# Performance work log

Measured on AMD Instinct MI355X. Metric: run time of the kernel, lower is better.

## Reference

```python
import jax, jax.numpy as jnp
import numpy as np

ALPHA = 0.2   # curvature threshold (init arg alpha)
BETA = 0.5    # ODE step weight (init arg beta)
BIG = 1e9     # sentinel used by torch.where(den < alpha, 1e9, den)


def setup_inputs() -> dict:
    key = jax.random.key(0)
    ks = jax.random.split(key, 6)
    B, N, D = 8, 128, 256
    return {
        "node_inputs": jax.random.normal(ks[0], (B * N, D), jnp.float32),
        "edges_input": jax.random.normal(ks[1], (B * N * N, D), jnp.float32),
        "W_n2e": jax.random.normal(ks[2], (2 * D, D), jnp.float32) * 0.05,
        "b_n2e": jnp.zeros((D,), jnp.float32),
        "W_e2v1": jax.random.normal(ks[3], (D, D // 2), jnp.float32) * 0.05,
        "b_e2v1": jnp.zeros((D // 2,), jnp.float32),
        "W_e2v2": jax.random.normal(ks[4], (D // 2, 1), jnp.float32) * 0.05,
        "b_e2v2": jnp.zeros((1,), jnp.float32),
        "num_atoms": N,
    }


def calc_k(e):
    # e: [B, N, N] nonnegative edge values (relu output).
    # Faithful vectorization of the torch nonzero/scatter/max code:
    # for each masked edge (i, j), denominator = max over row (i resp. j) where
    # entries < alpha OR at columns {i, j} are replaced by 1e9 (the scattered
    # zeros are < alpha so they also become 1e9). We get the exact row max
    # excluding columns {i, j} from the per-row top-3, then max with BIG.
    B, N, _ = e.shape
    mask = (e >= ALPHA) & (e < 1.0)
    r = jnp.where(e < ALPHA, BIG, e)                 # [B, N, N]
    vals, idx = jax.lax.top_k(r, 3)                   # [B, N, 3]
    ar = jnp.arange(N)
    # den_i: uses row i's top-k; exclude entries at columns i (dim 1) and j (dim 2)
    excl_i = (idx[:, :, None, :] == ar[None, :, None, None]) | \
             (idx[:, :, None, :] == ar[None, None, :, None])   # [B, N, N, 3]
    den_i = jnp.maximum(
        jnp.max(jnp.where(excl_i, -jnp.inf, vals[:, :, None, :]), axis=-1), BIG)
    # den_j: uses row j's top-k; same column exclusions
    excl_j = (idx[:, None, :, :] == ar[None, :, None, None]) | \
             (idx[:, None, :, :] == ar[None, None, :, None])
    den_j = jnp.maximum(
        jnp.max(jnp.where(excl_j, -jnp.inf, vals[:, None, :, :]), axis=-1), BIG)
    num = jnp.where(mask, e, 1.0)  # safe value where unmasked (sqrt-grad safety)
    s = jnp.sqrt(num / den_i) + jnp.sqrt(num / den_j)
    cur = jnp.where(mask, s, 0.0)
    return 2.0 - cur.reshape(-1)                      # [B*N*N]


def reference(node_inputs, edges_input, W_n2e, b_n2e, W_e2v1, b_e2v1,
              W_e2v2, b_e2v2, num_atoms):
    N = num_atoms
    D = node_inputs.shape[1]
    x = node_inputs.reshape(-1, N, D)                 # [B, N, D]
    # rel_send/rel_rec one-hot matmuls == direct gathers (row-major edge order)
    send = jnp.arange(N * N) // N
    rec = jnp.arange(N * N) % N
    edges = jnp.concatenate([x[:, send, :], x[:, rec, :]], axis=-1)  # [B, N*N, 2D]
    ez = jax.nn.gelu(edges @ W_n2e + b_n2e, approximate=False)       # [B, N*N, D]
    # dropout p=0.0 -> identity
    h = jax.nn.relu(ez @ W_e2v1 + b_e2v1)             # [B, N*N, D/2]
    e2v = jax.nn.relu((h @ W_e2v2 + b_e2v2)[..., 0])  # [B, N*N]
    ez_flat = ez.reshape(-1, D)                       # [B*N*N, D]
    k = calc_k(e2v.reshape(-1, N, N))[:, None]        # [B*N*N, 1], broadcast over D
    sig = jax.nn.sigmoid(ez_flat)
    grad1 = (k - jnp.exp(sig)) * edges_input
    return ez_flat + BETA * grad1, e2v
```

## Files before the change

### kernel.cpp

```cpp
#include <hip/hip_runtime.h>
#include <cmath>

typedef __attribute__((ext_vector_type(8))) short bf16x8;
typedef __attribute__((ext_vector_type(4))) float f32x4;
typedef unsigned short u16;
typedef unsigned int u32;

#define OUT1OFF 33554432

__device__ __forceinline__ u16 f2bf(float f) {
  union { float f; u32 u; } v; v.f = f;
  u32 r = v.u + 0x7fffu + ((v.u >> 16) & 1u);
  return (u16)(r >> 16);
}

__device__ __forceinline__ float frcp(float x) {
  float r;
  asm("v_rcp_f32 %0, %1" : "=v"(r) : "v"(x));
  return r;
}

__device__ __forceinline__ u32 cvt_pk_bf16(float lo, float hi) {
  u32 r;
  asm("v_cvt_pk_bf16_f32 %0, %1, %2" : "=v"(r) : "v"(lo), "v"(hi));
  return r;
}

__device__ __forceinline__ float gelu_t(float x) {
  const float x2 = x * x;
  const float z = 1.5957691216057308f * x * fmaf(0.044715f, x2, 1.0f);
  return x * frcp(1.0f + __expf(-z));
}

__global__ __launch_bounds__(256) void k1_prep(
    const float* __restrict__ x, const float* __restrict__ Wn2e,
    const float* __restrict__ bn2e, const float* __restrict__ W1,
    float* __restrict__ Uw, float* __restrict__ Yw, u16* __restrict__ W1F)
{
  __shared__ float xl[4][256];
  const int t = threadIdx.x;
  const int blk = blockIdx.x;
  const int r0 = blk * 4;
  {
    const int rr = t >> 6, c4 = (t & 63) * 4;
    *(float4*)&xl[rr][c4] = *(const float4*)&x[(r0 + rr) * 256 + c4];
  }
  __syncthreads();
  const int c = t;
  float u0=0.f,u1=0.f,u2=0.f,u3=0.f,y0=0.f,y1=0.f,y2=0.f,y3=0.f;
  #pragma unroll 4
  for (int k = 0; k < 256; ++k) {
    const float wt = Wn2e[k * 256 + c];
    const float wb = Wn2e[(k + 256) * 256 + c];
    const float a0 = xl[0][k], a1 = xl[1][k], a2 = xl[2][k], a3 = xl[3][k];
    u0 = fmaf(a0, wt, u0); u1 = fmaf(a1, wt, u1);
    u2 = fmaf(a2, wt, u2); u3 = fmaf(a3, wt, u3);
    y0 = fmaf(a0, wb, y0); y1 = fmaf(a1, wb, y1);
    y2 = fmaf(a2, wb, y2); y3 = fmaf(a3, wb, y3);
  }
  const float bb = bn2e[c];
  Uw[(r0+0)*256+c]=u0; Uw[(r0+1)*256+c]=u1; Uw[(r0+2)*256+c]=u2; Uw[(r0+3)*256+c]=u3;
  Yw[(r0+0)*256+c]=y0+bb; Yw[(r0+1)*256+c]=y1+bb; Yw[(r0+2)*256+c]=y2+bb; Yw[(r0+3)*256+c]=y3+bb;
  if (blk < 64) {
    #pragma unroll
    for (int q = 0; q < 2; ++q) {
      const int e = (blk * 256 + t) * 2 + q;
      const int d = e & 7, lf = (e >> 3) & 63, ks = (e >> 9) & 7, nt = (e >> 12) & 7;
      const int n = nt * 16 + (lf & 15);
      const int kg = ks * 32 + ((lf >> 4) & 3) * 8 + d;
      W1F[e] = f2bf(W1[kg * 128 + n]);
    }
  }
}

__global__ __launch_bounds__(256, 4) void k2_fused(
    const float* __restrict__ Uw, const float* __restrict__ Yw,
    const u16* __restrict__ W1F, const float* __restrict__ b1,
    const float* __restrict__ W2, const float* __restrict__ b2p,
    const float* __restrict__ E, float* __restrict__ out)
{
  __shared__ u16 ezLds[64 * 256];
  const int t = threadIdx.x;
  const int blk = blockIdx.x;
  const int pair = blk >> 1;
  const int j0 = (blk & 1) * 64;
  const int b = pair >> 7;
  const int rw = t >> 6;
  const int c4 = (t & 63) * 4;

  const float4 uv = *(const float4*)&Uw[pair * 256 + c4];

  #pragma unroll 4
  for (int it = 0; it < 16; ++it) {
    const int jj = it * 4 + rw;
    const int g = pair * 128 + j0 + jj;
    const float4 yv = *(const float4*)&Yw[(b * 128 + j0 + jj) * 256 + c4];
    const float4 ev = *(const float4*)&E[g * 256 + c4];
    const float ez0 = gelu_t(uv.x + yv.x);
    const float ez1 = gelu_t(uv.y + yv.y);
    const float ez2 = gelu_t(uv.z + yv.z);
    const float ez3 = gelu_t(uv.w + yv.w);
    uint2 pk;
    pk.x = cvt_pk_bf16(ez0, ez1);
    pk.y = cvt_pk_bf16(ez2, ez3);
    const int idx = (jj * 256 + c4) ^ ((jj & 7) << 3);
    *(uint2*)&ezLds[idx] = pk;
    float4 o;
    o.x = ez0 + (1.f - 0.5f * __expf(frcp(1.f + __expf(-ez0)))) * ev.x;
    o.y = ez1 + (1.f - 0.5f * __expf(frcp(1.f + __expf(-ez1)))) * ev.y;
    o.z = ez2 + (1.f - 0.5f * __expf(frcp(1.f + __expf(-ez2)))) * ev.z;
    o.w = ez3 + (1.f - 0.5f * __expf(frcp(1.f + __expf(-ez3)))) * ev.w;
    *(float4*)&out[g * 256 + c4] = o;
  }
  __syncthreads();

  const int l = t & 63;
  const int l15 = l & 15, lh = l >> 4;
  const int m0 = rw * 16;
  f32x4 acc[8];
  #pragma unroll
  for (int nt = 0; nt < 8; ++nt) acc[nt] = (f32x4){0.f, 0.f, 0.f, 0.f};
  #pragma unroll
  for (int ks = 0; ks < 8; ++ks) {
    const int k = ks * 32 + lh * 8;
    const int aidx = ((m0 + l15) * 256 + k) ^ ((l15 & 7) << 3);
    const bf16x8 a = *(const bf16x8*)&ezLds[aidx];
    #pragma unroll
    for (int nt = 0; nt < 8; ++nt) {
      const bf16x8 bv = *(const bf16x8*)&W1F[(((nt << 3) | ks) * 64 + l) * 8];
      acc[nt] = __builtin_amdgcn_mfma_f32_16x16x32_bf16(a, bv, acc[nt], 0, 0, 0);
    }
  }
  float ps0=0.f, ps1=0.f, ps2=0.f, ps3=0.f;
  #pragma unroll
  for (int nt = 0; nt < 8; ++nt) {
    const int col = nt * 16 + l15;
    const float bv = b1[col], wvv = W2[col];
    ps0 += fmaxf(acc[nt][0] + bv, 0.f) * wvv;
    ps1 += fmaxf(acc[nt][1] + bv, 0.f) * wvv;
    ps2 += fmaxf(acc[nt][2] + bv, 0.f) * wvv;
    ps3 += fmaxf(acc[nt][3] + bv, 0.f) * wvv;
  }
  #pragma unroll
  for (int m = 1; m < 16; m <<= 1) {
    ps0 += __shfl_xor(ps0, m, 64);
    ps1 += __shfl_xor(ps1, m, 64);
    ps2 += __shfl_xor(ps2, m, 64);
    ps3 += __shfl_xor(ps3, m, 64);
  }
  const float b2 = b2p[0];
  const float e0 = fmaxf(ps0 + b2, 0.f);
  const float e1 = fmaxf(ps1 + b2, 0.f);
  const float e2 = fmaxf(ps2 + b2, 0.f);
  const float e3 = fmaxf(ps3 + b2, 0.f);
  const int srcLane = ((l15 >> 2) << 4) | l15;
  const float s0 = __shfl(e0, srcLane, 64);
  const float s1 = __shfl(e1, srcLane, 64);
  const float s2 = __shfl(e2, srcLane, 64);
  const float s3 = __shfl(e3, srcLane, 64);
  const float t01 = (l15 & 1) ? s1 : s0;
  const float t23 = (l15 & 1) ? s3 : s2;
  const float s = (l15 & 2) ? t23 : t01;
  if (l < 16) out[OUT1OFF + pair * 128 + j0 + m0 + l] = s;
}

extern "C" void kernel_launch(void* const* d_in, const int* in_sizes, int n_in,
                              void* d_out, int out_size, void* d_ws, size_t ws_size,
                              hipStream_t stream) {
  const float* x    = (const float*)d_in[0];
  const float* E    = (const float*)d_in[1];
  const float* Wn2e = (const float*)d_in[2];
  const float* bn2e = (const float*)d_in[3];
  const float* W1   = (const float*)d_in[4];
  const float* b1   = (const float*)d_in[5];
  const float* W2   = (const float*)d_in[6];
  const float* b2   = (const float*)d_in[7];
  float* out = (float*)d_out;

  float* Uw = (float*)d_ws;
  float* Yw = Uw + 262144;
  u16*  W1F = (u16*)(Yw + 262144);

  hipLaunchKernelGGL(k1_prep, dim3(256), dim3(256), 0, stream,
                     x, Wn2e, bn2e, W1, Uw, Yw, W1F);
  hipLaunchKernelGGL(k2_fused, dim3(2048), dim3(256), 0, stream,
                     Uw, Yw, W1F, b1, W2, b2, E, out);
}
```

Before: 83.04 us.

## Halve k2 block tile to 32 rows, split MFMA N across waves, nontemporal stores

```diff
diff --git a/kernel.cpp b/kernel.cpp
--- a/kernel.cpp
+++ b/kernel.cpp
@@ -73,29 +73,32 @@
   }
 }
 
-__global__ __launch_bounds__(256, 4) void k2_fused(
+__global__ __launch_bounds__(256, 8) void k2_fused(
     const float* __restrict__ Uw, const float* __restrict__ Yw,
     const u16* __restrict__ W1F, const float* __restrict__ b1,
     const float* __restrict__ W2, const float* __restrict__ b2p,
     const float* __restrict__ E, float* __restrict__ out)
 {
-  __shared__ u16 ezLds[64 * 256];
+  __shared__ u16 ezLds[32 * 256];
+  __shared__ float psumBuf[2][32];
   const int t = threadIdx.x;
   const int blk = blockIdx.x;
-  const int pair = blk >> 1;
-  const int j0 = (blk & 1) * 64;
+  const int pair = blk >> 2;
+  const int j0 = (blk & 3) * 32;
   const int b = pair >> 7;
   const int rw = t >> 6;
-  const int c4 = (t & 63) * 4;
+  const int l = t & 63;
+  const int c4 = l * 4;
 
-  const float4 uv = *(const float4*)&Uw[pair * 256 + c4];
+  const f32x4 uv = *(const f32x4*)&Uw[pair * 256 + c4];
+  const int eBase = (pair * 128 + j0) * 256 + c4;
+  const int yBase = (b * 128 + j0) * 256 + c4;
 
-  #pragma unroll 4
-  for (int it = 0; it < 16; ++it) {
+  #pragma unroll 2
+  for (int it = 0; it < 8; ++it) {
     const int jj = it * 4 + rw;
-    const int g = pair * 128 + j0 + jj;
-    const float4 yv = *(const float4*)&Yw[(b * 128 + j0 + jj) * 256 + c4];
-    const float4 ev = *(const float4*)&E[g * 256 + c4];
+    const f32x4 yv = *(const f32x4*)&Yw[yBase + jj * 256];
+    const f32x4 ev = *(const f32x4*)&E[eBase + jj * 256];
     const float ez0 = gelu_t(uv.x + yv.x);
     const float ez1 = gelu_t(uv.y + yv.y);
     const float ez2 = gelu_t(uv.z + yv.z);
@@ -105,36 +108,37 @@
     pk.y = cvt_pk_bf16(ez2, ez3);
     const int idx = (jj * 256 + c4) ^ ((jj & 7) << 3);
     *(uint2*)&ezLds[idx] = pk;
-    float4 o;
+    f32x4 o;
     o.x = ez0 + (1.f - 0.5f * __expf(frcp(1.f + __expf(-ez0)))) * ev.x;
     o.y = ez1 + (1.f - 0.5f * __expf(frcp(1.f + __expf(-ez1)))) * ev.y;
     o.z = ez2 + (1.f - 0.5f * __expf(frcp(1.f + __expf(-ez2)))) * ev.z;
     o.w = ez3 + (1.f - 0.5f * __expf(frcp(1.f + __expf(-ez3)))) * ev.w;
-    *(float4*)&out[g * 256 + c4] = o;
+    __builtin_nontemporal_store(o, (f32x4*)&out[eBase + jj * 256]);
   }
   __syncthreads();
 
-  const int l = t & 63;
   const int l15 = l & 15, lh = l >> 4;
-  const int m0 = rw * 16;
-  f32x4 acc[8];
+  const int mrow = (rw >> 1) * 16;
+  const int nh = rw & 1;
+  f32x4 acc[4];
   #pragma unroll
-  for (int nt = 0; nt < 8; ++nt) acc[nt] = (f32x4){0.f, 0.f, 0.f, 0.f};
+  for (int nt = 0; nt < 4; ++nt) acc[nt] = (f32x4){0.f, 0.f, 0.f, 0.f};
   #pragma unroll
   for (int ks = 0; ks < 8; ++ks) {
     const int k = ks * 32 + lh * 8;
-    const int aidx = ((m0 + l15) * 256 + k) ^ ((l15 & 7) << 3);
+    const int aidx = ((mrow + l15) * 256 + k) ^ ((l15 & 7) << 3);
     const bf16x8 a = *(const bf16x8*)&ezLds[aidx];
     #pragma unroll
-    for (int nt = 0; nt < 8; ++nt) {
-      const bf16x8 bv = *(const bf16x8*)&W1F[(((nt << 3) | ks) * 64 + l) * 8];
+    for (int nt = 0; nt < 4; ++nt) {
+      const int ntg = nh * 4 + nt;
+      const bf16x8 bv = *(const bf16x8*)&W1F[(((ntg << 3) | ks) * 64 + l) * 8];
       acc[nt] = __builtin_amdgcn_mfma_f32_16x16x32_bf16(a, bv, acc[nt], 0, 0, 0);
     }
   }
   float ps0=0.f, ps1=0.f, ps2=0.f, ps3=0.f;
   #pragma unroll
-  for (int nt = 0; nt < 8; ++nt) {
-    const int col = nt * 16 + l15;
+  for (int nt = 0; nt < 4; ++nt) {
+    const int col = nh * 64 + nt * 16 + l15;
     const float bv = b1[col], wvv = W2[col];
     ps0 += fmaxf(acc[nt][0] + bv, 0.f) * wvv;
     ps1 += fmaxf(acc[nt][1] + bv, 0.f) * wvv;
@@ -148,20 +152,22 @@
     ps2 += __shfl_xor(ps2, m, 64);
     ps3 += __shfl_xor(ps3, m, 64);
   }
-  const float b2 = b2p[0];
-  const float e0 = fmaxf(ps0 + b2, 0.f);
-  const float e1 = fmaxf(ps1 + b2, 0.f);
-  const float e2 = fmaxf(ps2 + b2, 0.f);
-  const float e3 = fmaxf(ps3 + b2, 0.f);
-  const int srcLane = ((l15 >> 2) << 4) | l15;
-  const float s0 = __shfl(e0, srcLane, 64);
-  const float s1 = __shfl(e1, srcLane, 64);
-  const float s2 = __shfl(e2, srcLane, 64);
-  const float s3 = __shfl(e3, srcLane, 64);
-  const float t01 = (l15 & 1) ? s1 : s0;
-  const float t23 = (l15 & 1) ? s3 : s2;
-  const float s = (l15 & 2) ? t23 : t01;
-  if (l < 16) out[OUT1OFF + pair * 128 + j0 + m0 + l] = s;
+  {
+    const int srcLane = ((l15 >> 2) << 4) | l15;
+    const float s0 = __shfl(ps0, srcLane, 64);
+    const float s1 = __shfl(ps1, srcLane, 64);
+    const float s2 = __shfl(ps2, srcLane, 64);
+    const float s3 = __shfl(ps3, srcLane, 64);
+    const float t01 = (l15 & 1) ? s1 : s0;
+    const float t23 = (l15 & 1) ? s3 : s2;
+    const float s = (l15 & 2) ? t23 : t01;
+    if (l < 16) psumBuf[nh][mrow + l] = s;
+  }
+  __syncthreads();
+  if (t < 32) {
+    const float s = fmaxf(psumBuf[0][t] + psumBuf[1][t] + b2p[0], 0.f);
+    out[OUT1OFF + pair * 128 + j0 + t] = s;
+  }
 }
 
 extern "C" void kernel_launch(void* const* d_in, const int* in_sizes, int n_in,
@@ -183,6 +189,6 @@
 
   hipLaunchKernelGGL(k1_prep, dim3(256), dim3(256), 0, stream,
                      x, Wn2e, bn2e, W1, Uw, Yw, W1F);
-  hipLaunchKernelGGL(k2_fused, dim3(2048), dim3(256), 0, stream,
+  hipLaunchKernelGGL(k2_fused, dim3(4096), dim3(256), 0, stream,
                      Uw, Yw, W1F, b1, W2, b2, E, out);
 }
```

Result: faster. 75.82 us (-8.7%).
